# Kernel optimization log

Hardware: AMD Instinct MI355X
Metric: run time of the kernel (lower is better)

## Reference

```python
import jax, jax.numpy as jnp
import numpy as np

N_NODES = 100000


def gcn_conv(x, src, dst, deg_inv_sqrt, W, b):
    # x: [N, Fin], src/dst: [E_total] (self-loops included), W: [Fin, Fout]
    h = x @ W                                  # [N, Fout]
    norm = deg_inv_sqrt[src] * deg_inv_sqrt[dst]  # [E_total]
    msgs = h[src] * norm[:, None]              # [E_total, Fout] gather
    out = jax.ops.segment_sum(msgs, dst, num_segments=N_NODES)  # scatter-add
    return out + b


def setup_inputs() -> dict:
    key = jax.random.key(0)
    k1, k2, k3, k4, k5, k6, k7, k8 = jax.random.split(key, 8)
    input_dim, hidden_dim, out_dim = 4, 64, 2
    n_edges = 3200000
    x = jax.random.normal(k1, (N_NODES, input_dim), dtype=jnp.float32)
    edge_index = jax.random.randint(k2, (2, n_edges), 0, N_NODES, dtype=jnp.int64)
    s1 = 1.0 / np.sqrt(input_dim)
    s2 = 1.0 / np.sqrt(hidden_dim)
    W1 = jax.random.uniform(k3, (input_dim, hidden_dim), jnp.float32, -s1, s1)
    b1 = jnp.zeros((hidden_dim,), jnp.float32)
    W2 = jax.random.uniform(k4, (hidden_dim, hidden_dim), jnp.float32, -s2, s2)
    b2 = jnp.zeros((hidden_dim,), jnp.float32)
    Wf = jax.random.uniform(k5, (hidden_dim, out_dim), jnp.float32, -s2, s2)
    bf = jax.random.uniform(k6, (out_dim,), jnp.float32, -s2, s2)
    return {"x": x, "edge_index": edge_index, "W1": W1, "b1": b1,
            "W2": W2, "b2": b2, "Wf": Wf, "bf": bf}


def reference(x, edge_index, W1, b1, W2, b2, Wf, bf):
    # Add self-loops (PyG GCNConv default)
    loop = jnp.arange(N_NODES, dtype=edge_index.dtype)
    src = jnp.concatenate([edge_index[0], loop])
    dst = jnp.concatenate([edge_index[1], loop])
    # Symmetric normalization: degree on destination after self-loops
    deg = jax.ops.segment_sum(jnp.ones_like(dst, dtype=x.dtype), dst,
                              num_segments=N_NODES)
    deg_inv_sqrt = jnp.where(deg > 0, jax.lax.rsqrt(deg), 0.0)
    h = jax.nn.relu(gcn_conv(x, src, dst, deg_inv_sqrt, W1, b1))
    h = jax.nn.relu(gcn_conv(h, src, dst, deg_inv_sqrt, W2, b2))
    return h @ Wf + bf
```

## Files before the change

### kernel.cpp

```cpp
#include <hip/hip_runtime.h>
#include <hip/hip_bf16.h>

#define N_NODES 100000
#define N_EDGES 3200000
#define NB ((N_NODES + 255) / 256)
#define NBUCKET NB
#define EPB 8192
#define NPB ((N_EDGES + EPB - 1) / EPB)
#define BCAP 11264

__device__ inline unsigned f2bf(float f) {
  unsigned x = __float_as_uint(f);
  return (x + 0x7FFFu + ((x >> 16) & 1u)) >> 16;
}


__global__ void __launch_bounds__(256) k_pass1(const int* __restrict__ src,
                                               const int* __restrict__ dst,
                                               int* __restrict__ gcur,
                                               unsigned int* __restrict__ eb) {
  __shared__ int hist[NBUCKET];
  __shared__ int gbase[NBUCKET];
  int tid = threadIdx.x;
  int base = blockIdx.x * EPB;
  int cnt = min(EPB, N_EDGES - base);
  int n4 = cnt >> 2;
  for (int i = tid; i < NBUCKET; i += 256) hist[i] = 0;
  __syncthreads();
  const int4* d4 = (const int4*)(dst + base);
  const int4* s4 = (const int4*)(src + base);
  unsigned mv[32];
  unsigned short mb[32];
#pragma unroll
  for (int k = 0; k < 8; ++k) {
    int i = tid + (k << 8);
    if (i < n4) {
      int4 dv = d4[i];
      int4 sv = s4[i];
      int b0 = dv.x >> 8, b1_ = dv.y >> 8, b2 = dv.z >> 8, b3 = dv.w >> 8;
      unsigned p0 = atomicAdd(&hist[b0], 1);
      unsigned p1 = atomicAdd(&hist[b1_], 1);
      unsigned p2 = atomicAdd(&hist[b2], 1);
      unsigned p3 = atomicAdd(&hist[b3], 1);
      mv[4 * k + 0] = (unsigned)sv.x | ((unsigned)(dv.x & 255) << 17) | (p0 << 25);
      mv[4 * k + 1] = (unsigned)sv.y | ((unsigned)(dv.y & 255) << 17) | (p1 << 25);
      mv[4 * k + 2] = (unsigned)sv.z | ((unsigned)(dv.z & 255) << 17) | (p2 << 25);
      mv[4 * k + 3] = (unsigned)sv.w | ((unsigned)(dv.w & 255) << 17) | (p3 << 25);
      mb[4 * k + 0] = (unsigned short)b0;
      mb[4 * k + 1] = (unsigned short)b1_;
      mb[4 * k + 2] = (unsigned short)b2;
      mb[4 * k + 3] = (unsigned short)b3;
    } else {
      mb[4 * k + 0] = 0xFFFF; mb[4 * k + 1] = 0xFFFF;
      mb[4 * k + 2] = 0xFFFF; mb[4 * k + 3] = 0xFFFF;
    }
  }
  __syncthreads();
  for (int b = tid; b < NBUCKET; b += 256) {
    int h = hist[b];
    gbase[b] = h ? atomicAdd(&gcur[b], h) : 0;
  }
  __syncthreads();
#pragma unroll
  for (int k = 0; k < 32; ++k) {
    if (mb[k] != 0xFFFF) {
      int b = mb[k];
      unsigned v = mv[k];
      unsigned pos = (unsigned)gbase[b] + (v >> 25);
      if (pos < BCAP) eb[(size_t)b * BCAP + pos] = v & 0x01FFFFFFu;
    }
  }
}


__global__ void __launch_bounds__(256) k_part2(unsigned int* __restrict__ eb,
                                               const int* __restrict__ gcur,
                                               int* __restrict__ rs, int* __restrict__ re,
                                               float* __restrict__ dis,
                                               const float4* __restrict__ x4,
                                               float4* __restrict__ xd) {
  __shared__ int hist[256], scn[256], cur[256];
  __shared__ int tot;
  __shared__ unsigned int stage[BCAP];
  int b = blockIdx.x, tid = threadIdx.x;
  int n0 = b << 8;
  int cnt = gcur[b];
  int base = b * BCAP;
  hist[tid] = 0; cur[tid] = 0;
  __syncthreads();
  for (int i = tid; i < cnt; i += 256)
    atomicAdd(&hist[eb[base + i] >> 17], 1);
  __syncthreads();
  int n = n0 + tid;
  int deg = hist[tid];
  int slots = (n < N_NODES) ? ((deg + 1 + 7) & ~7) : 0;
  int x = slots;
  scn[tid] = x;
  __syncthreads();
  for (int off = 1; off < 256; off <<= 1) {
    int t = (tid >= off) ? scn[tid - off] : 0;
    __syncthreads();
    x += t; scn[tid] = x;
    __syncthreads();
  }
  int excl = x - slots;
  if (tid == 255) tot = x;
  if (n < N_NODES) {
    rs[n]  = base + excl;
    re[n]  = base + excl + deg + 1;
    float dn = rsqrtf((float)(deg + 1));
    dis[n] = dn;
    float4 xv = x4[n];
    float4 w; w.x = xv.x * dn; w.y = xv.y * dn; w.z = xv.z * dn; w.w = xv.w * dn;
    xd[n] = w;
    stage[excl] = (unsigned)n;
    for (int i = deg + 1; i < slots; ++i)
      stage[excl + i] = (unsigned)N_NODES;
  }
  if (b == 0 && tid == 0) xd[N_NODES] = make_float4(0.f, 0.f, 0.f, 0.f);
  scn[tid] = excl + 1;
  __syncthreads();
  for (int i = tid; i < cnt; i += 256) {
    unsigned v = eb[base + i];
    unsigned low = v >> 17;
    int lpos = scn[low] + atomicAdd(&cur[low], 1);
    stage[lpos] = v & 0x1FFFFu;
  }
  __syncthreads();
  int total = tot;
  for (int i = tid; i < total; i += 256)
    eb[base + i] = stage[i];
  if (tid < 16) {
    int gp = total + tid;
    if (gp < BCAP) eb[base + gp] = (unsigned)N_NODES;
  }
}


__global__ void __launch_bounds__(256) k_l1(const float4* __restrict__ xd,
                                            const float* __restrict__ dis,
                                            const int* __restrict__ rs,
                                            const int* __restrict__ re,
                                            const int* __restrict__ csr,
                                            const float* __restrict__ W1,
                                            const float* __restrict__ b1,
                                            unsigned int* __restrict__ h1o) {
  int gt = blockIdx.x * 256 + threadIdx.x;
  int nid = gt >> 2, p = gt & 3;
  if (nid > N_NODES) return;
  if (nid == N_NODES) {
    uint4 z = make_uint4(0u, 0u, 0u, 0u);
    uint4* op = (uint4*)(h1o + nid * 32 + p * 8);
    op[0] = z; op[1] = z;
    return;
  }
  int e0 = rs[nid];
  int it4 = ((re[nid] - e0 + 7) & ~7) >> 2;
  const int* cp = csr + e0 + p;
  float ax = 0.f, ay = 0.f, az = 0.f, aw = 0.f;
#pragma unroll 4
  for (int t = 0; t < it4; ++t) {
    int s = cp[t << 2];
    float4 v = xd[s];
    ax += v.x; ay += v.y; az += v.z; aw += v.w;
  }
  ax += __shfl_xor(ax, 1); ax += __shfl_xor(ax, 2);
  ay += __shfl_xor(ay, 1); ay += __shfl_xor(ay, 2);
  az += __shfl_xor(az, 1); az += __shfl_xor(az, 2);
  aw += __shfl_xor(aw, 1); aw += __shfl_xor(aw, 2);
  float dn = dis[nid];
  ax *= dn; ay *= dn; az *= dn; aw *= dn;
  int j0 = p << 4;
  unsigned ou[8];
#pragma unroll
  for (int j2 = 0; j2 < 8; ++j2) {
    int j = j0 + j2 * 2;
    float s0 = b1[j]     + ax * W1[j]     + ay * W1[64 + j]     + az * W1[128 + j]     + aw * W1[192 + j];
    float s1 = b1[j + 1] + ax * W1[j + 1] + ay * W1[64 + j + 1] + az * W1[128 + j + 1] + aw * W1[192 + j + 1];
    unsigned u0 = f2bf(fmaxf(s0, 0.f) * dn);
    unsigned u1 = f2bf(fmaxf(s1, 0.f) * dn);
    ou[j2] = u0 | (u1 << 16);
  }
  uint4* op = (uint4*)(h1o + nid * 32 + p * 8);
  op[0] = make_uint4(ou[0], ou[1], ou[2], ou[3]);
  op[1] = make_uint4(ou[4], ou[5], ou[6], ou[7]);
}


__device__ inline void acc_bf2(float& a0, float& a1, unsigned u) {
  a0 += __uint_as_float(u << 16);
  a1 += __uint_as_float(u & 0xffff0000u);
}

__global__ void __launch_bounds__(256)
k_layer2(const __hip_bfloat16* __restrict__ h1s, const float* __restrict__ dis,
         const int* __restrict__ rs, const int* __restrict__ re,
         const int* __restrict__ csr,
         const float* __restrict__ W2, const float* __restrict__ b2,
         const float* __restrict__ Wf, const float* __restrict__ bf,
         float* __restrict__ out) {
  __shared__ float sh[4][64];
  int l = threadIdx.x & 63;
  int w = threadIdx.x >> 6;
  int n = blockIdx.x * 4 + w;
  int g = l >> 3;
  int c = l & 7;

  const unsigned int* h32 = (const unsigned int*)h1s;
  int e0 = rs[n];
  int iter = (re[n] - e0 + 7) >> 3;
  const int* cb = csr + e0 + g;
  int coff = c << 2;

  float a0 = 0.f, a1 = 0.f, a2 = 0.f, a3 = 0.f;
  float a4 = 0.f, a5 = 0.f, a6 = 0.f, a7 = 0.f;
  int sc = cb[0];
  int sn = cb[8];
  uint4 u = *(const uint4*)(h32 + (sc << 5) + coff);
  for (int it = 1; it < iter; ++it) {
    int sf = cb[(it + 1) << 3];
    uint4 r = *(const uint4*)(h32 + (sn << 5) + coff);
    acc_bf2(a0, a1, u.x); acc_bf2(a2, a3, u.y);
    acc_bf2(a4, a5, u.z); acc_bf2(a6, a7, u.w);
    u = r; sn = sf;
  }
  acc_bf2(a0, a1, u.x); acc_bf2(a2, a3, u.y);
  acc_bf2(a4, a5, u.z); acc_bf2(a6, a7, u.w);

#define RED3(a) a += __shfl_xor(a, 8); a += __shfl_xor(a, 16); a += __shfl_xor(a, 32);
  RED3(a0) RED3(a1) RED3(a2) RED3(a3) RED3(a4) RED3(a5) RED3(a6) RED3(a7)
#undef RED3

  float dn = dis[n];
  if (l < 8) {
    float4 v0; v0.x = a0 * dn; v0.y = a1 * dn; v0.z = a2 * dn; v0.w = a3 * dn;
    float4 v1; v1.x = a4 * dn; v1.y = a5 * dn; v1.z = a6 * dn; v1.w = a7 * dn;
    *(float4*)&sh[w][(l << 3) + 0] = v0;
    *(float4*)&sh[w][(l << 3) + 4] = v1;
  }
  __syncthreads();

  float t = b2[l];
  const float4* shv = (const float4*)sh[w];
#pragma unroll 4
  for (int j4 = 0; j4 < 16; ++j4) {
    float4 a4v = shv[j4];
    t += a4v.x * W2[(4 * j4 + 0) * 64 + l];
    t += a4v.y * W2[(4 * j4 + 1) * 64 + l];
    t += a4v.z * W2[(4 * j4 + 2) * 64 + l];
    t += a4v.w * W2[(4 * j4 + 3) * 64 + l];
  }
  t = fmaxf(t, 0.0f);

  float p0 = t * Wf[l * 2 + 0];
  float p1 = t * Wf[l * 2 + 1];
  for (int off = 32; off; off >>= 1) {
    p0 += __shfl_down(p0, off);
    p1 += __shfl_down(p1, off);
  }
  if (l == 0) {
    out[n * 2 + 0] = p0 + bf[0];
    out[n * 2 + 1] = p1 + bf[1];
  }
}


extern "C" void kernel_launch(void* const* d_in, const int* in_sizes, int n_in,
                              void* d_out, int out_size, void* d_ws, size_t ws_size,
                              hipStream_t stream) {
  const float* x  = (const float*)d_in[0];
  const int*   ei = (const int*)d_in[1];
  const float* W1 = (const float*)d_in[2];
  const float* b1 = (const float*)d_in[3];
  const float* W2 = (const float*)d_in[4];
  const float* b2 = (const float*)d_in[5];
  const float* Wf = (const float*)d_in[6];
  const float* bf = (const float*)d_in[7];
  float* out = (float*)d_out;

  const int* srcv = ei;
  const int* dstv = ei + N_EDGES;

  char* p = (char*)d_ws;
  auto take = [&](size_t bytes) { char* r = p; p += (bytes + 255) & ~(size_t)255; return r; };
  int*          gcur = (int*)take((size_t)NBUCKET * 4);
  unsigned int* eb   = (unsigned int*)take((size_t)NBUCKET * BCAP * 4 + 512);
  int*          rs   = (int*)take((size_t)N_NODES * 4);
  int*          re   = (int*)take((size_t)N_NODES * 4);
  float*        dis  = (float*)take((size_t)N_NODES * 4);
  float4*       xd   = (float4*)take((size_t)(N_NODES + 1) * 16);
  __hip_bfloat16* h1s = (__hip_bfloat16*)take((size_t)(N_NODES + 1) * 64 * 2);

  (void)hipMemsetAsync(gcur, 0, (size_t)NBUCKET * 4, stream);
  k_pass1<<<NPB, 256, 0, stream>>>(srcv, dstv, gcur, eb);
  k_part2<<<NBUCKET, 256, 0, stream>>>(eb, gcur, rs, re, dis, (const float4*)x, xd);
  const int* csr = (const int*)eb;
  k_l1<<<((N_NODES + 1) * 4 + 255) / 256, 256, 0, stream>>>(xd, dis, rs, re, csr, W1, b1, (unsigned int*)h1s);
  k_layer2<<<N_NODES / 4, 256, 0, stream>>>(h1s, dis, rs, re, csr, W2, b2, Wf, bf, out);
}
```

Baseline: 245.3 us.

## Split layer-2 into aggregation kernel and persistent register-weight GEMV kernel

Splits the fused layer-2 kernel in two. k_agg does only the neighbor gather-sum, using a two-deep prefetch pipeline, and writes fp32 aggregates to a new 25.6MB workspace buffer. k_final runs as a persistent grid in which each wave keeps a column of W2 in registers and broadcasts the aggregate values with readlane, which removes the per-node W2 reloads and the shared-memory __syncthreads. The cost is an extra global round-trip for the aggregates, one more kernel launch, and higher register use.

```diff
diff --git a/kernel.cpp b/kernel.cpp
--- a/kernel.cpp
+++ b/kernel.cpp
@@ -8,6 +8,8 @@
 #define EPB 8192
 #define NPB ((N_EDGES + EPB - 1) / EPB)
 #define BCAP 11264
+#define KF_BLOCKS 1280
+#define KF_WAVES (KF_BLOCKS * 4)
 
 __device__ inline unsigned f2bf(float f) {
   unsigned x = __float_as_uint(f);
@@ -193,13 +195,9 @@
 }
 
 __global__ void __launch_bounds__(256)
-k_layer2(const __hip_bfloat16* __restrict__ h1s, const float* __restrict__ dis,
-         const int* __restrict__ rs, const int* __restrict__ re,
-         const int* __restrict__ csr,
-         const float* __restrict__ W2, const float* __restrict__ b2,
-         const float* __restrict__ Wf, const float* __restrict__ bf,
-         float* __restrict__ out) {
-  __shared__ float sh[4][64];
+k_agg(const __hip_bfloat16* __restrict__ h1s, const float* __restrict__ dis,
+      const int* __restrict__ rs, const int* __restrict__ re,
+      const int* __restrict__ csr, float* __restrict__ agg) {
   int l = threadIdx.x & 63;
   int w = threadIdx.x >> 6;
   int n = blockIdx.x * 4 + w;
@@ -214,18 +212,21 @@
 
   float a0 = 0.f, a1 = 0.f, a2 = 0.f, a3 = 0.f;
   float a4 = 0.f, a5 = 0.f, a6 = 0.f, a7 = 0.f;
-  int sc = cb[0];
-  int sn = cb[8];
-  uint4 u = *(const uint4*)(h32 + (sc << 5) + coff);
-  for (int it = 1; it < iter; ++it) {
-    int sf = cb[(it + 1) << 3];
-    uint4 r = *(const uint4*)(h32 + (sn << 5) + coff);
-    acc_bf2(a0, a1, u.x); acc_bf2(a2, a3, u.y);
-    acc_bf2(a4, a5, u.z); acc_bf2(a6, a7, u.w);
-    u = r; sn = sf;
-  }
-  acc_bf2(a0, a1, u.x); acc_bf2(a2, a3, u.y);
-  acc_bf2(a4, a5, u.z); acc_bf2(a6, a7, u.w);
+
+  int s0 = cb[0];
+  int s1 = (iter > 1) ? cb[8] : N_NODES;
+  uint4 u0 = *(const uint4*)(h32 + (s0 << 5) + coff);
+  uint4 u1 = *(const uint4*)(h32 + (s1 << 5) + coff);
+  int sc2 = cb[16];
+#pragma unroll 2
+  for (int it = 0; it < iter; ++it) {
+    int ss = (it + 2 < iter) ? sc2 : N_NODES;
+    uint4 r = *(const uint4*)(h32 + (ss << 5) + coff);
+    sc2 = cb[(it + 3) << 3];
+    acc_bf2(a0, a1, u0.x); acc_bf2(a2, a3, u0.y);
+    acc_bf2(a4, a5, u0.z); acc_bf2(a6, a7, u0.w);
+    u0 = u1; u1 = r;
+  }
 
 #define RED3(a) a += __shfl_xor(a, 8); a += __shfl_xor(a, 16); a += __shfl_xor(a, 32);
   RED3(a0) RED3(a1) RED3(a2) RED3(a3) RED3(a4) RED3(a5) RED3(a6) RED3(a7)
@@ -235,32 +236,58 @@
   if (l < 8) {
     float4 v0; v0.x = a0 * dn; v0.y = a1 * dn; v0.z = a2 * dn; v0.w = a3 * dn;
     float4 v1; v1.x = a4 * dn; v1.y = a5 * dn; v1.z = a6 * dn; v1.w = a7 * dn;
-    *(float4*)&sh[w][(l << 3) + 0] = v0;
-    *(float4*)&sh[w][(l << 3) + 4] = v1;
-  }
-  __syncthreads();
-
-  float t = b2[l];
-  const float4* shv = (const float4*)sh[w];
-#pragma unroll 4
-  for (int j4 = 0; j4 < 16; ++j4) {
-    float4 a4v = shv[j4];
-    t += a4v.x * W2[(4 * j4 + 0) * 64 + l];
-    t += a4v.y * W2[(4 * j4 + 1) * 64 + l];
-    t += a4v.z * W2[(4 * j4 + 2) * 64 + l];
-    t += a4v.w * W2[(4 * j4 + 3) * 64 + l];
-  }
-  t = fmaxf(t, 0.0f);
-
-  float p0 = t * Wf[l * 2 + 0];
-  float p1 = t * Wf[l * 2 + 1];
-  for (int off = 32; off; off >>= 1) {
-    p0 += __shfl_down(p0, off);
-    p1 += __shfl_down(p1, off);
-  }
-  if (l == 0) {
-    out[n * 2 + 0] = p0 + bf[0];
-    out[n * 2 + 1] = p1 + bf[1];
+    float4* ap = (float4*)(agg + (size_t)n * 64 + (l << 3));
+    ap[0] = v0; ap[1] = v1;
+  }
+}
+
+
+__global__ void __launch_bounds__(256)
+k_final(const float* __restrict__ agg, const float* __restrict__ W2,
+        const float* __restrict__ b2, const float* __restrict__ Wf,
+        const float* __restrict__ bf, float* __restrict__ out) {
+  int l = threadIdx.x & 63;
+  int w = threadIdx.x >> 6;
+  int wv = blockIdx.x * 4 + w;
+
+  float wcol[64];
+#pragma unroll
+  for (int j = 0; j < 64; ++j) wcol[j] = W2[j * 64 + l];
+  float bias = b2[l];
+  float wf0 = Wf[l * 2 + 0];
+  float wf1 = Wf[l * 2 + 1];
+  float bf0 = bf[0], bf1 = bf[1];
+
+  int n = wv;
+  float av = agg[(size_t)n * 64 + l];
+  while (true) {
+    int n2 = n + KF_WAVES;
+    float anext = 0.f;
+    if (n2 < N_NODES) anext = agg[(size_t)n2 * 64 + l];
+
+    unsigned ub = __float_as_uint(av);
+    float t0 = bias, t1 = 0.f, t2 = 0.f, t3 = 0.f;
+#pragma unroll
+    for (int j = 0; j < 64; j += 4) {
+      t0 = fmaf(__uint_as_float(__builtin_amdgcn_readlane(ub, j + 0)), wcol[j + 0], t0);
+      t1 = fmaf(__uint_as_float(__builtin_amdgcn_readlane(ub, j + 1)), wcol[j + 1], t1);
+      t2 = fmaf(__uint_as_float(__builtin_amdgcn_readlane(ub, j + 2)), wcol[j + 2], t2);
+      t3 = fmaf(__uint_as_float(__builtin_amdgcn_readlane(ub, j + 3)), wcol[j + 3], t3);
+    }
+    float t = fmaxf((t0 + t1) + (t2 + t3), 0.f);
+
+    float p0 = t * wf0;
+    float p1 = t * wf1;
+    for (int off = 32; off; off >>= 1) {
+      p0 += __shfl_down(p0, off);
+      p1 += __shfl_down(p1, off);
+    }
+    if (l == 0) {
+      out[n * 2 + 0] = p0 + bf0;
+      out[n * 2 + 1] = p1 + bf1;
+    }
+    if (n2 >= N_NODES) break;
+    av = anext; n = n2;
   }
 }
 
@@ -290,11 +317,13 @@
   float*        dis  = (float*)take((size_t)N_NODES * 4);
   float4*       xd   = (float4*)take((size_t)(N_NODES + 1) * 16);
   __hip_bfloat16* h1s = (__hip_bfloat16*)take((size_t)(N_NODES + 1) * 64 * 2);
+  float*        agg  = (float*)take((size_t)N_NODES * 64 * 4);
 
   (void)hipMemsetAsync(gcur, 0, (size_t)NBUCKET * 4, stream);
   k_pass1<<<NPB, 256, 0, stream>>>(srcv, dstv, gcur, eb);
   k_part2<<<NBUCKET, 256, 0, stream>>>(eb, gcur, rs, re, dis, (const float4*)x, xd);
   const int* csr = (const int*)eb;
   k_l1<<<((N_NODES + 1) * 4 + 255) / 256, 256, 0, stream>>>(xd, dis, rs, re, csr, W1, b1, (unsigned int*)h1s);
-  k_layer2<<<N_NODES / 4, 256, 0, stream>>>(h1s, dis, rs, re, csr, W2, b2, Wf, bf, out);
-}
+  k_agg<<<N_NODES / 4, 256, 0, stream>>>(h1s, dis, rs, re, csr, agg);
+  k_final<<<KF_BLOCKS, 256, 0, stream>>>(agg, W2, b2, Wf, bf, out);
+}
```

Result: faster. 239.2 us (-2.5%).

## Split layer-2 into aggregation and per-node dense GEMV kernels; warp-shuffle scan

Applied to the files above, without the earlier changes.

Layer 2 is split into two kernels. The first only aggregates neighbour features and writes them to a 25.6 MB fp32 buffer. The second has each thread compute the full 64x64 W2 product plus the final projection for one node, from a swizzled shared-memory tile, instead of every 64-lane wave doing a serialized dot product per node after the gather. The block prefix scan in partitioning now uses wave shuffles instead of a barrier-heavy shared-memory scan. The trade is an extra global round trip of the aggregated features, one more launch, and a 64-float register array per thread with 64 KB of shared memory per block, which may limit occupancy.

```diff
diff --git a/kernel.cpp b/kernel.cpp
--- a/kernel.cpp
+++ b/kernel.cpp
@@ -8,6 +8,7 @@
 #define EPB 8192
 #define NPB ((N_EDGES + EPB - 1) / EPB)
 #define BCAP 11264
+#define KF_BLOCKS ((N_NODES + 255) / 256)
 
 __device__ inline unsigned f2bf(float f) {
   unsigned x = __float_as_uint(f);
@@ -80,9 +81,11 @@
                                                const float4* __restrict__ x4,
                                                float4* __restrict__ xd) {
   __shared__ int hist[256], scn[256], cur[256];
+  __shared__ int wsum[4];
   __shared__ int tot;
   __shared__ unsigned int stage[BCAP];
   int b = blockIdx.x, tid = threadIdx.x;
+  int lane = tid & 63, wid = tid >> 6;
   int n0 = b << 8;
   int cnt = gcur[b];
   int base = b * BCAP;
@@ -94,15 +97,18 @@
   int n = n0 + tid;
   int deg = hist[tid];
   int slots = (n < N_NODES) ? ((deg + 1 + 7) & ~7) : 0;
-  int x = slots;
-  scn[tid] = x;
-  __syncthreads();
-  for (int off = 1; off < 256; off <<= 1) {
-    int t = (tid >= off) ? scn[tid - off] : 0;
-    __syncthreads();
-    x += t; scn[tid] = x;
-    __syncthreads();
-  }
+  int v = slots;
+#pragma unroll
+  for (int off = 1; off < 64; off <<= 1) {
+    int t = __shfl_up(v, off);
+    if (lane >= off) v += t;
+  }
+  if (lane == 63) wsum[wid] = v;
+  __syncthreads();
+  int x = v;
+#pragma unroll
+  for (int w2 = 0; w2 < 3; ++w2)
+    if (wid > w2) x += wsum[w2];
   int excl = x - slots;
   if (tid == 255) tot = x;
   if (n < N_NODES) {
@@ -121,10 +127,10 @@
   scn[tid] = excl + 1;
   __syncthreads();
   for (int i = tid; i < cnt; i += 256) {
-    unsigned v = eb[base + i];
-    unsigned low = v >> 17;
+    unsigned v2 = eb[base + i];
+    unsigned low = v2 >> 17;
     int lpos = scn[low] + atomicAdd(&cur[low], 1);
-    stage[lpos] = v & 0x1FFFFu;
+    stage[lpos] = v2 & 0x1FFFFu;
   }
   __syncthreads();
   int total = tot;
@@ -193,13 +199,9 @@
 }
 
 __global__ void __launch_bounds__(256)
-k_layer2(const __hip_bfloat16* __restrict__ h1s, const float* __restrict__ dis,
-         const int* __restrict__ rs, const int* __restrict__ re,
-         const int* __restrict__ csr,
-         const float* __restrict__ W2, const float* __restrict__ b2,
-         const float* __restrict__ Wf, const float* __restrict__ bf,
-         float* __restrict__ out) {
-  __shared__ float sh[4][64];
+k_agg(const __hip_bfloat16* __restrict__ h1s, const float* __restrict__ dis,
+      const int* __restrict__ rs, const int* __restrict__ re,
+      const int* __restrict__ csr, float* __restrict__ agg) {
   int l = threadIdx.x & 63;
   int w = threadIdx.x >> 6;
   int n = blockIdx.x * 4 + w;
@@ -235,32 +237,57 @@
   if (l < 8) {
     float4 v0; v0.x = a0 * dn; v0.y = a1 * dn; v0.z = a2 * dn; v0.w = a3 * dn;
     float4 v1; v1.x = a4 * dn; v1.y = a5 * dn; v1.z = a6 * dn; v1.w = a7 * dn;
-    *(float4*)&sh[w][(l << 3) + 0] = v0;
-    *(float4*)&sh[w][(l << 3) + 4] = v1;
-  }
-  __syncthreads();
-
-  float t = b2[l];
-  const float4* shv = (const float4*)sh[w];
-#pragma unroll 4
-  for (int j4 = 0; j4 < 16; ++j4) {
-    float4 a4v = shv[j4];
-    t += a4v.x * W2[(4 * j4 + 0) * 64 + l];
-    t += a4v.y * W2[(4 * j4 + 1) * 64 + l];
-    t += a4v.z * W2[(4 * j4 + 2) * 64 + l];
-    t += a4v.w * W2[(4 * j4 + 3) * 64 + l];
-  }
-  t = fmaxf(t, 0.0f);
-
-  float p0 = t * Wf[l * 2 + 0];
-  float p1 = t * Wf[l * 2 + 1];
-  for (int off = 32; off; off >>= 1) {
-    p0 += __shfl_down(p0, off);
-    p1 += __shfl_down(p1, off);
-  }
-  if (l == 0) {
-    out[n * 2 + 0] = p0 + bf[0];
-    out[n * 2 + 1] = p1 + bf[1];
+    float4* ap = (float4*)(agg + (size_t)n * 64 + (l << 3));
+    ap[0] = v0; ap[1] = v1;
+  }
+}
+
+
+__global__ void __launch_bounds__(256)
+k_final(const float* __restrict__ agg, const float* __restrict__ W2,
+        const float* __restrict__ b2, const float* __restrict__ Wf,
+        const float* __restrict__ bf, float* __restrict__ out) {
+  __shared__ float sa[256 * 64];
+  int tid = threadIdx.x;
+  int l = tid & 63;
+  int w = tid >> 6;
+  int n0 = blockIdx.x * 256;
+
+#pragma unroll 8
+  for (int i = 0; i < 64; ++i) {
+    int row = (w << 6) + i;
+    int n = n0 + row;
+    float v = (n < N_NODES) ? agg[(size_t)n * 64 + l] : 0.f;
+    sa[(row << 6) + (l ^ (row & 31))] = v;
+  }
+  __syncthreads();
+
+  int nl = (w << 6) + l;
+  int n = n0 + nl;
+  const float* sr = sa + (nl << 6);
+  int sw = nl & 31;
+
+  float t[64];
+#pragma unroll
+  for (int k = 0; k < 64; ++k) t[k] = b2[k];
+#pragma unroll 2
+  for (int j = 0; j < 64; ++j) {
+    float v = sr[j ^ sw];
+#pragma unroll
+    for (int k = 0; k < 64; ++k)
+      t[k] = fmaf(v, W2[(j << 6) + k], t[k]);
+  }
+
+  float p0 = bf[0], p1 = bf[1];
+#pragma unroll
+  for (int k = 0; k < 64; ++k) {
+    float tv = fmaxf(t[k], 0.f);
+    p0 = fmaf(tv, Wf[k * 2 + 0], p0);
+    p1 = fmaf(tv, Wf[k * 2 + 1], p1);
+  }
+  if (n < N_NODES) {
+    out[n * 2 + 0] = p0;
+    out[n * 2 + 1] = p1;
   }
 }
 
@@ -290,11 +317,13 @@
   float*        dis  = (float*)take((size_t)N_NODES * 4);
   float4*       xd   = (float4*)take((size_t)(N_NODES + 1) * 16);
   __hip_bfloat16* h1s = (__hip_bfloat16*)take((size_t)(N_NODES + 1) * 64 * 2);
+  float*        agg  = (float*)take((size_t)N_NODES * 64 * 4);
 
   (void)hipMemsetAsync(gcur, 0, (size_t)NBUCKET * 4, stream);
   k_pass1<<<NPB, 256, 0, stream>>>(srcv, dstv, gcur, eb);
   k_part2<<<NBUCKET, 256, 0, stream>>>(eb, gcur, rs, re, dis, (const float4*)x, xd);
   const int* csr = (const int*)eb;
   k_l1<<<((N_NODES + 1) * 4 + 255) / 256, 256, 0, stream>>>(xd, dis, rs, re, csr, W1, b1, (unsigned int*)h1s);
-  k_layer2<<<N_NODES / 4, 256, 0, stream>>>(h1s, dis, rs, re, csr, W2, b2, Wf, bf, out);
-}
+  k_agg<<<N_NODES / 4, 256, 0, stream>>>(h1s, dis, rs, re, csr, agg);
+  k_final<<<KF_BLOCKS, 256, 0, stream>>>(agg, W2, b2, Wf, bf, out);
+}
```

After: 258.0 us. 1.05x slower.
